# Kernel tuning notes

Measured on AMD Instinct MI355X. Metric: run time of the kernel, lower is better.

The kernel has to match this reference:

```python
import jax, jax.numpy as jnp
import numpy as np

N_EMBD = 1024
N_HEAD = 16
HEAD = N_EMBD // N_HEAD


def setup_inputs() -> dict:
    key = jax.random.key(0)
    k1, k2, k3 = jax.random.split(key, 3)
    x = jax.random.normal(k1, (2, 2048, N_EMBD), dtype=jnp.float32)
    # torch Linear weight is [out, in]; store transposed for x @ W
    W_attn = jax.random.normal(k2, (N_EMBD, 3 * N_EMBD), dtype=jnp.float32) * (1.0 / np.sqrt(N_EMBD))
    W_proj = jax.random.normal(k3, (N_EMBD, N_EMBD), dtype=jnp.float32) * (1.0 / np.sqrt(N_EMBD))
    return {"x": x, "W_attn": W_attn, "W_proj": W_proj}


def reference(x, W_attn, W_proj):
    B, T, C = x.shape
    qkv = x @ W_attn  # [B,T,3C]
    q, k, v = jnp.split(qkv, 3, axis=-1)
    # [B,T,H,D] -> [B,H,T,D]
    q = q.reshape(B, T, N_HEAD, HEAD).transpose(0, 2, 1, 3)
    k = k.reshape(B, T, N_HEAD, HEAD).transpose(0, 2, 1, 3)
    v = v.reshape(B, T, N_HEAD, HEAD).transpose(0, 2, 1, 3)
    att = jnp.einsum('bhqd,bhkd->bhqk', q, k) * (1.0 / np.sqrt(HEAD))
    causal = jnp.tril(jnp.ones((T, T), dtype=bool))
    att = jnp.where(causal[None, None], att, jnp.float32(-jnp.inf))
    att = jax.nn.softmax(att, axis=-1)
    y = jnp.einsum('bhqk,bhkd->bhqd', att, v)
    y = y.transpose(0, 2, 1, 3).reshape(B, T, C)
    return y @ W_proj
```

## Files before the change

kernel.cpp:

```cpp
#include <hip/hip_runtime.h>

typedef unsigned short u16;
typedef __bf16 bf16x8 __attribute__((ext_vector_type(8)));
typedef float f32x4 __attribute__((ext_vector_type(4)));

#define BB 2
#define TT 2048
#define CC 1024
#define HH 16
#define DD 64
#define MM (BB*TT)

__device__ __forceinline__ u16 f2b(float f) {
    union { float f; unsigned int i; } a; a.f = f;
    unsigned int u = a.i;
    unsigned int r = (u + 0x7FFFu + ((u >> 16) & 1u)) >> 16;
    return (u16)r;
}
__device__ __forceinline__ u16 f2b_fast(float f) {
    union { float f; unsigned int i; } a; a.f = f;
    return (u16)((a.i + 0x8000u) >> 16);
}

__device__ __forceinline__ void gld16(const u16* g, u16* l) {
    __builtin_amdgcn_global_load_lds(
        (const __attribute__((address_space(1))) unsigned int*)g,
        (__attribute__((address_space(3))) unsigned int*)l, 16, 0, 0);
}

__global__ __launch_bounds__(256) void prep_k(const float* __restrict__ x,
                                              u16* __restrict__ xb,
                                              const float* __restrict__ Wa,
                                              u16* __restrict__ Wat,
                                              const float* __restrict__ Wp,
                                              u16* __restrict__ Wpt) {
    __shared__ u16 tile[64][65];
    const int b = blockIdx.x;
    const int tid = threadIdx.x;
    if (b < 4096) {
        int i = b * 256 + tid;
        float4 v = ((const float4*)x)[i];
        ushort4 o;
        o.x = f2b(v.x); o.y = f2b(v.y); o.z = f2b(v.z); o.w = f2b(v.w);
        ((ushort4*)xb)[i] = o;
        return;
    }
    const float* in; u16* out; int K, N, n0, k0;
    if (b < 4096 + 768) {
        int bb = b - 4096;
        in = Wa; out = Wat; K = 1024; N = 3072;
        n0 = (bb % 48) * 64; k0 = (bb / 48) * 64;
    } else {
        int bb = b - 4096 - 768;
        in = Wp; out = Wpt; K = 1024; N = 1024;
        n0 = (bb % 16) * 64; k0 = (bb / 16) * 64;
    }
    const int tx = tid & 63, ty = tid >> 6;
    for (int i = 0; i < 16; i++) {
        int row = ty + i * 4;
        tile[row][tx] = f2b(in[(size_t)(k0 + row) * N + n0 + tx]);
    }
    __syncthreads();
    for (int i = 0; i < 16; i++) {
        int row = ty + i * 4;
        out[(size_t)(n0 + row) * K + k0 + tx] = tile[tx][row];
    }
}

template<int MODE>
__global__ __launch_bounds__(256) void gemm_k(const u16* __restrict__ A,
                                              const u16* __restrict__ Bt,
                                              u16* __restrict__ Cq,
                                              u16* __restrict__ Ck,
                                              u16* __restrict__ Cv,
                                              float* __restrict__ Cout,
                                              int N, int K) {
    constexpr int BN   = (MODE == 0) ? 128 : 64;
    constexpr int NF   = (MODE == 0) ? 4 : 2;
    constexpr int BSU  = BN * 32;
    constexpr int LDSZ = (MODE == 0) ? (128 * 136) : (2 * 4096 + 2 * BSU);
    __shared__ __attribute__((aligned(16))) u16 smem[LDSZ];
#define AsP(B) (smem + (B) * 4096)
#define BsP(B) (smem + 8192 + (B) * BSU)

    const int tid  = threadIdx.x;
    const int lane = tid & 63, w = tid >> 6;
    const int wm = w >> 1, wn = w & 1;
    const int quad = lane >> 4, l16 = lane & 15;

    const int nwg = gridDim.x, lin = blockIdx.x;
    const int cpx = nwg >> 3;
    const int sw  = (lin & 7) * cpx + (lin >> 3);
    const int ncols = N / BN;
    const int m0 = (sw / ncols) * 128, n0 = (sw % ncols) * BN;

    f32x4 acc[4][NF];
    for (int mi = 0; mi < 4; mi++)
        for (int ni = 0; ni < NF; ni++)
            for (int e = 0; e < 4; e++) acc[mi][ni][e] = 0.f;

#define GSTAGE(BUF, K0) do {                                                  \
    for (int i = 0; i < 2; i++) {                                             \
        int c = tid + 256 * i;                                                \
        int row = c >> 2, col = (c & 3) * 8;                                  \
        const u16* srcA;                                                      \
        if constexpr (MODE == 0) {                                            \
            srcA = A + (size_t)(m0 + row) * K + (K0) + col;                   \
        } else {                                                              \
            int m = m0 + row;                                                 \
            int b = m >> 11, t = m & 2047;                                    \
            int kk = (K0) + col;                                              \
            int h = kk >> 6, d = kk & 63;                                     \
            srcA = A + ((size_t)(b * HH + h) * TT + t) * DD + d;              \
        }                                                                     \
        gld16(srcA, AsP(BUF) + c * 8);                                        \
    }                                                                         \
    if constexpr (MODE == 0) {                                                \
        for (int i = 0; i < 2; i++) {                                         \
            int c = tid + 256 * i;                                            \
            int row = c >> 2, col = (c & 3) * 8;                              \
            gld16(Bt + (size_t)(n0 + row) * K + (K0) + col, BsP(BUF) + c * 8);\
        }                                                                     \
    } else {                                                                  \
        int row = tid >> 2, col = (tid & 3) * 8;                              \
        gld16(Bt + (size_t)(n0 + row) * K + (K0) + col, BsP(BUF) + tid * 8);  \
    }                                                                         \
} while (0)

    GSTAGE(0, 0);
    const int nk = K >> 5;
    for (int jk = 0; jk < nk; jk++) {
        const int cb = jk & 1;
        __syncthreads();
        if (jk + 1 < nk) { GSTAGE(cb ^ 1, (jk + 1) * 32); }
        bf16x8 af[4], bfm[NF];
        for (int mi = 0; mi < 4; mi++)
            af[mi] = *(const bf16x8*)(AsP(cb) + (wm * 64 + mi * 16 + l16) * 32 + quad * 8);
        for (int ni = 0; ni < NF; ni++)
            bfm[ni] = *(const bf16x8*)(BsP(cb) + ((BN / 2) * wn + ni * 16 + l16) * 32 + quad * 8);
        for (int mi = 0; mi < 4; mi++)
            for (int ni = 0; ni < NF; ni++)
                acc[mi][ni] = __builtin_amdgcn_mfma_f32_16x16x32_bf16(
                    af[mi], bfm[ni], acc[mi][ni], 0, 0, 0);
    }
#undef GSTAGE

    if constexpr (MODE == 0) {
        const float SCQ = 0.125f * 1.44269504f;
        const int which = n0 >> 10;
        if (which < 2) {
            for (int mi = 0; mi < 4; mi++)
                for (int ni = 0; ni < 4; ni++)
                    for (int r = 0; r < 4; r++) {
                        int row = m0 + wm * 64 + mi * 16 + quad * 4 + r;
                        int col = n0 + wn * 64 + ni * 16 + l16;
                        int h = (col >> 6) & 15, d = col & 63;
                        int b = row >> 11, t = row & 2047;
                        size_t off = ((size_t)(b * HH + h) * TT + t) * DD + d;
                        float val = acc[mi][ni][r];
                        if (which == 0) val *= SCQ;
                        (which == 0 ? Cq : Ck)[off] = f2b(val);
                    }
        } else {
            __syncthreads();
            for (int mi = 0; mi < 4; mi++)
                for (int ni = 0; ni < 4; ni++)
                    for (int r = 0; r < 4; r++) {
                        int cl = wn * 64 + ni * 16 + l16;
                        int tl = wm * 64 + mi * 16 + quad * 4 + r;
                        smem[cl * 136 + tl] = f2b(acc[mi][ni][r]);
                    }
            __syncthreads();
            const int b = m0 >> 11, t0l = m0 & 2047;
            const int c0 = n0 - 2048;
            for (int j = 0; j < 8; j++) {
                int idx = j * 256 + tid;
                int cl = idx >> 4, ch = idx & 15;
                int cg = c0 + cl, h = cg >> 6, d = cg & 63;
                uint4 val = *(const uint4*)&smem[cl * 136 + ch * 8];
                *(uint4*)&Cv[((size_t)(b * HH + h) * DD + d) * TT + t0l + ch * 8] = val;
            }
        }
    } else {
        for (int mi = 0; mi < 4; mi++)
            for (int ni = 0; ni < NF; ni++)
                for (int r = 0; r < 4; r++) {
                    int row = m0 + wm * 64 + mi * 16 + quad * 4 + r;
                    int col = n0 + wn * 32 + ni * 16 + l16;
                    Cout[(size_t)row * N + col] = acc[mi][ni][r];
                }
    }
#undef AsP
#undef BsP
}

__global__ __launch_bounds__(256, 2) void attn_k(const u16* __restrict__ Q,
                                                 const u16* __restrict__ Kb,
                                                 const u16* __restrict__ Vtg,
                                                 u16* __restrict__ Y) {
    __shared__ __attribute__((aligned(16))) u16 Ks[2][128 * 64];
    __shared__ __attribute__((aligned(16))) u16 Vs[2][64 * 128];
    __shared__ __attribute__((aligned(16))) u16 Ps[4][16 * 128];
    const int tid  = threadIdx.x;
    const int lane = tid & 63, w = tid >> 6;
    const int quad = lane >> 4, l16 = lane & 15;
    const int bh = blockIdx.x;
    const int y  = blockIdx.y;
    const int rowi = (y >> 1) & 3, coli = y >> 3;
    const int basew = ((coli & 1) ? 9 : 16) - ((coli >> 1) << 3);
    const int work = basew + ((coli & 1) ? rowi : -rowi);
    const int sb = 2 * (work - 1) + (y & 1);
    const int nkt = work;
    const size_t base  = (size_t)bh * TT * DD;
    const size_t baseV = (size_t)bh * DD * TT;

    int ksidx[4], koff[4], voff[4];
    for (int r = 0; r < 4; r++) {
        int sidx = r * 256 + tid;
        ksidx[r] = sidx;
        int kr = sidx >> 3, ksl = sidx & 7;
        koff[r] = kr * 64 + ((ksl ^ (kr & 7)) << 3);
        int vr = sidx >> 4, vsl = sidx & 15;
        voff[r] = vr * TT + ((vsl ^ (vr & 7)) << 3);
    }
    const u16* kg = Kb + base;
    const u16* vg = Vtg + baseV;

    for (int r = 0; r < 4; r++) gld16(kg + koff[r], &Ks[0][ksidx[r] * 8]);
    for (int r = 0; r < 4; r++) gld16(vg + voff[r], &Vs[0][ksidx[r] * 8]);

    bf16x8 qf[2];
    for (int kk = 0; kk < 2; kk++)
        qf[kk] = *(const bf16x8*)(Q + base +
            (size_t)(sb * 64 + w * 16 + l16) * DD + kk * 32 + quad * 8);

    const int swx = (l16 & 7);
    const int swk0 = ((quad ^ swx) << 3);
    const int swk1 = (((4 + quad) ^ swx) << 3);

    float mst[4], lst[4];
    f32x4 oacc[4];
    for (int r = 0; r < 4; r++) { mst[r] = -1e30f; lst[r] = 0.f; }
    for (int nd = 0; nd < 4; nd++)
        for (int e = 0; e < 4; e++) oacc[nd][e] = 0.f;

    for (int jk = 0; jk < nkt; jk++) {
        const int cb = jk & 1;
        __syncthreads();

        if (jk + 1 < nkt) {
            const u16* kn = kg + (size_t)(jk + 1) * (128 * DD);
            const u16* vn = vg + (size_t)(jk + 1) * 128;
            for (int r = 0; r < 4; r++)
                gld16(kn + koff[r], &Ks[cb ^ 1][ksidx[r] * 8]);
            for (int r = 0; r < 4; r++)
                gld16(vn + voff[r], &Vs[cb ^ 1][ksidx[r] * 8]);
        }

        f32x4 s[8];
        for (int ni = 0; ni < 8; ni++)
            for (int e = 0; e < 4; e++) s[ni][e] = 0.f;
        {
            bf16x8 kfa[8];
            for (int ni = 0; ni < 8; ni++)
                kfa[ni] = *(const bf16x8*)&Ks[cb][(ni * 16 + l16) * 64 + swk0];
            for (int ni = 0; ni < 8; ni++)
                s[ni] = __builtin_amdgcn_mfma_f32_16x16x32_bf16(
                    qf[0], kfa[ni], s[ni], 0, 0, 0);
        }
        {
            bf16x8 kfa[8];
            for (int ni = 0; ni < 8; ni++)
                kfa[ni] = *(const bf16x8*)&Ks[cb][(ni * 16 + l16) * 64 + swk1];
            for (int ni = 0; ni < 8; ni++)
                s[ni] = __builtin_amdgcn_mfma_f32_16x16x32_bf16(
                    qf[1], kfa[ni], s[ni], 0, 0, 0);
        }

        if (jk == (sb >> 1)) {
            int row0 = sb * 64 + w * 16 + quad * 4;
            int col0 = jk * 128 + l16;
            for (int ni = 0; ni < 8; ni++)
                for (int r = 0; r < 4; r++)
                    if (col0 + ni * 16 > row0 + r) s[ni][r] = -1e30f;
        }
        float alpha[4];
        for (int r = 0; r < 4; r++) {
            float mx = s[0][r];
            for (int ni = 1; ni < 8; ni++) mx = fmaxf(mx, s[ni][r]);
            for (int off = 8; off >= 1; off >>= 1)
                mx = fmaxf(mx, __shfl_xor(mx, off));
            float mn = fmaxf(mst[r], mx);
            alpha[r] = __builtin_amdgcn_exp2f(mst[r] - mn);
            mst[r] = mn;
        }
        float rs[4] = {0.f, 0.f, 0.f, 0.f};
        for (int ni = 0; ni < 8; ni++)
            for (int r = 0; r < 4; r++) {
                float pv = __builtin_amdgcn_exp2f(s[ni][r] - mst[r]);
                rs[r] += pv;
                int row = quad * 4 + r;
                int cg  = ni * 2 + (l16 >> 3);
                Ps[w][row * 128 + ((cg ^ row) << 3) + (l16 & 7)] = f2b_fast(pv);
            }
        for (int r = 0; r < 4; r++) {
            float sm = rs[r];
            for (int off = 8; off >= 1; off >>= 1)
                sm += __shfl_xor(sm, off);
            lst[r] = lst[r] * alpha[r] + sm;
            for (int nd = 0; nd < 4; nd++) oacc[nd][r] *= alpha[r];
        }

        for (int kk = 0; kk < 4; kk++) {
            const int swv = (((kk * 4 + quad) ^ swx) << 3);
            bf16x8 vfa[4];
            for (int nd = 0; nd < 4; nd++)
                vfa[nd] = *(const bf16x8*)&Vs[cb][(nd * 16 + l16) * 128 + swv];
            bf16x8 pf = *(const bf16x8*)&Ps[w][l16 * 128 +
                (((kk * 4 + quad) ^ l16) << 3)];
            for (int nd = 0; nd < 4; nd++)
                oacc[nd] = __builtin_amdgcn_mfma_f32_16x16x32_bf16(
                    pf, vfa[nd], oacc[nd], 0, 0, 0);
        }
    }

    for (int nd = 0; nd < 4; nd++)
        for (int r = 0; r < 4; r++) {
            int row = sb * 64 + w * 16 + quad * 4 + r;
            int col = nd * 16 + l16;
            Y[base + (size_t)row * DD + col] = f2b(oacc[nd][r] / lst[r]);
        }
}

extern "C" void kernel_launch(void* const* d_in, const int* in_sizes, int n_in,
                              void* d_out, int out_size, void* d_ws, size_t ws_size,
                              hipStream_t stream) {
    const float* x      = (const float*)d_in[0];
    const float* W_attn = (const float*)d_in[1];
    const float* W_proj = (const float*)d_in[2];
    float* out = (float*)d_out;

    u16* Wt_attn = (u16*)d_ws;
    u16* Wt_proj = Wt_attn + 3072 * 1024;
    u16* xb      = Wt_proj + 1024 * 1024;
    u16* q       = xb + (size_t)MM * CC;
    u16* k       = q + (size_t)32 * 2048 * 64;
    u16* vt      = k + (size_t)32 * 2048 * 64;
    u16* y       = vt + (size_t)32 * 2048 * 64;

    prep_k<<<dim3(4096 + 768 + 256), 256, 0, stream>>>(
        x, xb, W_attn, Wt_attn, W_proj, Wt_proj);
    gemm_k<0><<<dim3((MM / 128) * (3072 / 128)), 256, 0, stream>>>(
        xb, Wt_attn, q, k, vt, nullptr, 3072, 1024);
    attn_k<<<dim3(32, 32), 256, 0, stream>>>(q, k, vt, y);
    gemm_k<1><<<dim3((MM / 128) * (1024 / 64)), 256, 0, stream>>>(
        y, Wt_proj, nullptr, nullptr, nullptr, out, 1024, 1024);
}
```

Measured before the change: 181.1 us.

## Fuse x bf16 conversion into QKV GEMM load and single-buffer attention K/V

Removes the separate x-to-bf16 conversion pass and its workspace buffer by converting fp32 x inside the QKV GEMM's A-tile staging with vector loads and register stores to LDS. The attention kernel drops K/V double buffering, loading the next tile after compute behind an extra barrier, which halves K/V LDS use. This trades the async prefetch overlap and async A loads for less memory traffic on x and a smaller LDS footprint, at the cost of more fp32 reads of x across column tiles and exposed load latency.

```diff
diff --git a/kernel.cpp b/kernel.cpp
--- a/kernel.cpp
+++ b/kernel.cpp
@@ -28,30 +28,19 @@
         (__attribute__((address_space(3))) unsigned int*)l, 16, 0, 0);
 }
 
-__global__ __launch_bounds__(256) void prep_k(const float* __restrict__ x,
-                                              u16* __restrict__ xb,
-                                              const float* __restrict__ Wa,
+__global__ __launch_bounds__(256) void prep_k(const float* __restrict__ Wa,
                                               u16* __restrict__ Wat,
                                               const float* __restrict__ Wp,
                                               u16* __restrict__ Wpt) {
     __shared__ u16 tile[64][65];
     const int b = blockIdx.x;
     const int tid = threadIdx.x;
-    if (b < 4096) {
-        int i = b * 256 + tid;
-        float4 v = ((const float4*)x)[i];
-        ushort4 o;
-        o.x = f2b(v.x); o.y = f2b(v.y); o.z = f2b(v.z); o.w = f2b(v.w);
-        ((ushort4*)xb)[i] = o;
-        return;
-    }
     const float* in; u16* out; int K, N, n0, k0;
-    if (b < 4096 + 768) {
-        int bb = b - 4096;
+    if (b < 768) {
         in = Wa; out = Wat; K = 1024; N = 3072;
-        n0 = (bb % 48) * 64; k0 = (bb / 48) * 64;
+        n0 = (b % 48) * 64; k0 = (b / 48) * 64;
     } else {
-        int bb = b - 4096 - 768;
+        int bb = b - 768;
         in = Wp; out = Wpt; K = 1024; N = 1024;
         n0 = (bb % 16) * 64; k0 = (bb / 16) * 64;
     }
@@ -68,7 +57,8 @@
 }
 
 template<int MODE>
-__global__ __launch_bounds__(256) void gemm_k(const u16* __restrict__ A,
+__global__ __launch_bounds__(256) void gemm_k(const float* __restrict__ Axf,
+                                              const u16* __restrict__ A,
                                               const u16* __restrict__ Bt,
                                               u16* __restrict__ Cq,
                                               u16* __restrict__ Ck,
@@ -103,17 +93,24 @@
     for (int i = 0; i < 2; i++) {                                             \
         int c = tid + 256 * i;                                                \
         int row = c >> 2, col = (c & 3) * 8;                                  \
-        const u16* srcA;                                                      \
         if constexpr (MODE == 0) {                                            \
-            srcA = A + (size_t)(m0 + row) * K + (K0) + col;                   \
+            const float* sa = Axf + (size_t)(m0 + row) * K + (K0) + col;      \
+            float4 fa = ((const float4*)sa)[0];                               \
+            float4 fb = ((const float4*)sa)[1];                               \
+            bf16x8 vv;                                                        \
+            vv[0] = (__bf16)fa.x; vv[1] = (__bf16)fa.y;                       \
+            vv[2] = (__bf16)fa.z; vv[3] = (__bf16)fa.w;                       \
+            vv[4] = (__bf16)fb.x; vv[5] = (__bf16)fb.y;                       \
+            vv[6] = (__bf16)fb.z; vv[7] = (__bf16)fb.w;                       \
+            *(bf16x8*)(AsP(BUF) + c * 8) = vv;                                \
         } else {                                                              \
             int m = m0 + row;                                                 \
             int b = m >> 11, t = m & 2047;                                    \
             int kk = (K0) + col;                                              \
             int h = kk >> 6, d = kk & 63;                                     \
-            srcA = A + ((size_t)(b * HH + h) * TT + t) * DD + d;              \
+            gld16(A + ((size_t)(b * HH + h) * TT + t) * DD + d,               \
+                  AsP(BUF) + c * 8);                                          \
         }                                                                     \
-        gld16(srcA, AsP(BUF) + c * 8);                                        \
     }                                                                         \
     if constexpr (MODE == 0) {                                                \
         for (int i = 0; i < 2; i++) {                                         \
@@ -198,8 +195,8 @@
                                                  const u16* __restrict__ Kb,
                                                  const u16* __restrict__ Vtg,
                                                  u16* __restrict__ Y) {
-    __shared__ __attribute__((aligned(16))) u16 Ks[2][128 * 64];
-    __shared__ __attribute__((aligned(16))) u16 Vs[2][64 * 128];
+    __shared__ __attribute__((aligned(16))) u16 Ks[128 * 64];
+    __shared__ __attribute__((aligned(16))) u16 Vs[64 * 128];
     __shared__ __attribute__((aligned(16))) u16 Ps[4][16 * 128];
     const int tid  = threadIdx.x;
     const int lane = tid & 63, w = tid >> 6;
@@ -226,8 +223,8 @@
     const u16* kg = Kb + base;
     const u16* vg = Vtg + baseV;
 
-    for (int r = 0; r < 4; r++) gld16(kg + koff[r], &Ks[0][ksidx[r] * 8]);
-    for (int r = 0; r < 4; r++) gld16(vg + voff[r], &Vs[0][ksidx[r] * 8]);
+    for (int r = 0; r < 4; r++) gld16(kg + koff[r], &Ks[ksidx[r] * 8]);
+    for (int r = 0; r < 4; r++) gld16(vg + voff[r], &Vs[ksidx[r] * 8]);
 
     bf16x8 qf[2];
     for (int kk = 0; kk < 2; kk++)
@@ -245,17 +242,7 @@
         for (int e = 0; e < 4; e++) oacc[nd][e] = 0.f;
 
     for (int jk = 0; jk < nkt; jk++) {
-        const int cb = jk & 1;
         __syncthreads();
-
-        if (jk + 1 < nkt) {
-            const u16* kn = kg + (size_t)(jk + 1) * (128 * DD);
-            const u16* vn = vg + (size_t)(jk + 1) * 128;
-            for (int r = 0; r < 4; r++)
-                gld16(kn + koff[r], &Ks[cb ^ 1][ksidx[r] * 8]);
-            for (int r = 0; r < 4; r++)
-                gld16(vn + voff[r], &Vs[cb ^ 1][ksidx[r] * 8]);
-        }
 
         f32x4 s[8];
         for (int ni = 0; ni < 8; ni++)
@@ -263,7 +250,7 @@
         {
             bf16x8 kfa[8];
             for (int ni = 0; ni < 8; ni++)
-                kfa[ni] = *(const bf16x8*)&Ks[cb][(ni * 16 + l16) * 64 + swk0];
+                kfa[ni] = *(const bf16x8*)&Ks[(ni * 16 + l16) * 64 + swk0];
             for (int ni = 0; ni < 8; ni++)
                 s[ni] = __builtin_amdgcn_mfma_f32_16x16x32_bf16(
                     qf[0], kfa[ni], s[ni], 0, 0, 0);
@@ -271,7 +258,7 @@
         {
             bf16x8 kfa[8];
             for (int ni = 0; ni < 8; ni++)
-                kfa[ni] = *(const bf16x8*)&Ks[cb][(ni * 16 + l16) * 64 + swk1];
+                kfa[ni] = *(const bf16x8*)&Ks[(ni * 16 + l16) * 64 + swk1];
             for (int ni = 0; ni < 8; ni++)
                 s[ni] = __builtin_amdgcn_mfma_f32_16x16x32_bf16(
                     qf[1], kfa[ni], s[ni], 0, 0, 0);
@@ -315,12 +302,22 @@
             const int swv = (((kk * 4 + quad) ^ swx) << 3);
             bf16x8 vfa[4];
             for (int nd = 0; nd < 4; nd++)
-                vfa[nd] = *(const bf16x8*)&Vs[cb][(nd * 16 + l16) * 128 + swv];
+                vfa[nd] = *(const bf16x8*)&Vs[(nd * 16 + l16) * 128 + swv];
             bf16x8 pf = *(const bf16x8*)&Ps[w][l16 * 128 +
                 (((kk * 4 + quad) ^ l16) << 3)];
             for (int nd = 0; nd < 4; nd++)
                 oacc[nd] = __builtin_amdgcn_mfma_f32_16x16x32_bf16(
                     pf, vfa[nd], oacc[nd], 0, 0, 0);
+        }
+
+        if (jk + 1 < nkt) {
+            __syncthreads();
+            const u16* kn = kg + (size_t)(jk + 1) * (128 * DD);
+            const u16* vn = vg + (size_t)(jk + 1) * 128;
+            for (int r = 0; r < 4; r++)
+                gld16(kn + koff[r], &Ks[ksidx[r] * 8]);
+            for (int r = 0; r < 4; r++)
+                gld16(vn + voff[r], &Vs[ksidx[r] * 8]);
         }
     }
 
@@ -342,17 +339,15 @@
 
     u16* Wt_attn = (u16*)d_ws;
     u16* Wt_proj = Wt_attn + 3072 * 1024;
-    u16* xb      = Wt_proj + 1024 * 1024;
-    u16* q       = xb + (size_t)MM * CC;
+    u16* q       = Wt_proj + 1024 * 1024;
     u16* k       = q + (size_t)32 * 2048 * 64;
     u16* vt      = k + (size_t)32 * 2048 * 64;
     u16* y       = vt + (size_t)32 * 2048 * 64;
 
-    prep_k<<<dim3(4096 + 768 + 256), 256, 0, stream>>>(
-        x, xb, W_attn, Wt_attn, W_proj, Wt_proj);
+    prep_k<<<dim3(768 + 256), 256, 0, stream>>>(W_attn, Wt_attn, W_proj, Wt_proj);
     gemm_k<0><<<dim3((MM / 128) * (3072 / 128)), 256, 0, stream>>>(
-        xb, Wt_attn, q, k, vt, nullptr, 3072, 1024);
+        x, nullptr, Wt_attn, q, k, vt, nullptr, 3072, 1024);
     attn_k<<<dim3(32, 32), 256, 0, stream>>>(q, k, vt, y);
     gemm_k<1><<<dim3((MM / 128) * (1024 / 64)), 256, 0, stream>>>(
-        y, Wt_proj, nullptr, nullptr, nullptr, out, 1024, 1024);
-}
+        nullptr, y, Wt_proj, nullptr, nullptr, nullptr, out, 1024, 1024);
+}
```

Result: slower. 187.7 us (+3.7%).
